# Performance work log

Measured on AMD Instinct MI355X. Metric: run time of the kernel, lower is better.

Reference implementation:

```python
import jax, jax.numpy as jnp
import numpy as np

B, C, L = 16, 64, 512
L_P = 16
D_MODEL = 1024
STRIDE = 8
N_P = (L - L_P) // STRIDE + 2  # 64 patches
PERIOD = L // 2                # statsmodels period = series_input_length / 2


def setup_inputs() -> dict:
    key = jax.random.key(0)
    ks = jax.random.split(key, 11)
    s = 0.02  # small init scale for weights
    return {
        "data_x": jax.random.normal(ks[0], (B, C, L), jnp.float32),
        "gamma": jax.random.uniform(ks[1], (B, C, L), jnp.float32),
        "beta": jax.random.uniform(ks[2], (B, C, L), jnp.float32),
        "w_trend": jax.random.normal(ks[3], (L_P, L), jnp.float32) * s,
        "b_trend": jax.random.normal(ks[4], (L_P,), jnp.float32) * s,
        "w_seasonal": jax.random.normal(ks[5], (L_P, L), jnp.float32) * s,
        "b_seasonal": jax.random.normal(ks[6], (L_P,), jnp.float32) * s,
        "w_resid": jax.random.normal(ks[7], (L_P, L), jnp.float32) * s,
        "b_resid": jax.random.normal(ks[8], (L_P,), jnp.float32) * s,
        "w_g": jax.random.normal(ks[9], (D_MODEL, 3 * L_P), jnp.float32) * s,
        "b_g": jax.random.normal(ks[10], (D_MODEL,), jnp.float32) * s,
    }


def _decompose(x):
    """Vectorized statsmodels seasonal_decompose(model='additive', period=L//2).

    trend: centered moving average with filter [0.5,1,...,1,0.5]/p (even period),
           NaN edges -> replaced by 0 (as in the torch module).
    seasonal: per-phase nanmean of detrended, demeaned, tiled to length L.
    resid: detrended - seasonal on the valid (non-NaN) region, 0 elsewhere.
    x: [B, C, L] -> (trend, seasonal, resid) each [B, C, L].
    """
    p = PERIOD
    filt = jnp.concatenate([jnp.full((1,), 0.5, x.dtype),
                            jnp.ones((p - 1,), x.dtype),
                            jnp.full((1,), 0.5, x.dtype)]) / p  # len p+1 (p even)
    head = p // 2               # leading NaN count (filter is symmetric)
    nvalid = L - p              # valid trend samples
    xf = x.reshape(B * C, 1, L)
    tv = jax.lax.conv_general_dilated(xf, filt.reshape(1, 1, p + 1),
                                      (1,), "VALID")[:, 0, :]  # [BC, L-p]
    trend = jnp.zeros((B * C, L), x.dtype).at[:, head:head + nvalid].set(tv)
    dv = x.reshape(B * C, L)[:, head:head + nvalid] - tv  # detrended, valid region
    # per-phase nanmean over valid detrended samples
    phase = (head + jnp.arange(nvalid)) % p               # phase of each valid index
    sums = jnp.zeros((B * C, p), x.dtype).at[:, phase].add(dv)
    counts = jnp.zeros((p,), x.dtype).at[phase].add(1.0)
    pa = sums / counts                                    # period averages [BC, p]
    pa = pa - jnp.mean(pa, axis=1, keepdims=True)
    seasonal = jnp.tile(pa, (1, L // p))                  # L = 2p exactly
    resid = jnp.zeros((B * C, L), x.dtype).at[:, head:head + nvalid].set(
        dv - seasonal[:, head:head + nvalid])
    return (trend.reshape(B, C, L), seasonal.reshape(B, C, L),
            resid.reshape(B, C, L))


def reference(data_x, gamma, beta, w_trend, b_trend, w_seasonal, b_seasonal,
              w_resid, b_resid, w_g, b_g):
    # 'transformed': per-channel stats (dim=1), torch var is unbiased (ddof=1), epsi=0
    mean = jnp.mean(data_x, axis=1)
    var = jnp.var(data_x, axis=1, ddof=1)
    mean = (mean / jnp.sqrt(var))[:, None, :]             # [B,1,L] broadcast over C
    x = gamma * (data_x - mean) + beta
    x = jax.lax.stop_gradient(x)                          # season() detaches
    trend, seasonal, resid = _decompose(x)
    t = trend @ w_trend.T + b_trend                       # [B,C,L_p]
    s = seasonal @ w_seasonal.T + b_seasonal
    r = resid @ w_resid.T + b_resid
    feats = jnp.concatenate([t, s, r], axis=-1)           # [B,C,3*L_p]
    feats = jnp.broadcast_to(feats[:, :, None, :], (B, C, N_P, 3 * L_P))
    return feats @ w_g.T + b_g                            # [B,C,N_p,D_MODEL]
```

## Files before the change

### kernel.cpp

```cpp
#include <hip/hip_runtime.h>
#include <math.h>

#define BB   16
#define CC   64
#define LL   512
#define LP   16
#define DM   1024
#define NP   64
#define PRD  256
#define HEAD 128
#define NV   256

typedef float f32x4 __attribute__((ext_vector_type(4)));

#define OFF_MEANP 0
#define OFF_WSF   8192
#define OFF_WRS   12288
#define OFF_WGT   12304

__global__ __launch_bounds__(256) void statsprep_kernel(
    const float* __restrict__ dx, const float* __restrict__ w_s,
    const float* __restrict__ w_r, const float* __restrict__ w_g,
    float* __restrict__ ws)
{
    const int tid = threadIdx.x, bid = blockIdx.x;
    if (bid < 32) {
        int id = bid * 256 + tid;
        int b = id >> 9, l = id & 511;
        const float* p = dx + (size_t)b * CC * LL + l;
        float s = 0.f, sq = 0.f;
#pragma unroll 8
        for (int c = 0; c < CC; ++c) {
            float v = p[(size_t)c * LL];
            s += v; sq += v * v;
        }
        float mean = s * (1.0f / CC);
        float var  = (sq - (float)CC * mean * mean) * (1.0f / (CC - 1));
        ws[OFF_MEANP + id] = mean / sqrtf(var);
    } else if (bid == 32) {
#pragma unroll
        for (int idx = tid; idx < 16 * PRD; idx += 256) {
            int g = idx >> 8, m = idx & 255;
            ws[OFF_WSF + idx] = w_s[g * LL + m] + w_s[g * LL + PRD + m];
        }
        int g = tid >> 4, ln = tid & 15;
        float s = 0.f;
        for (int k = ln; k < PRD; k += 16) s += w_r[g * LL + HEAD + k];
#pragma unroll
        for (int m = 8; m; m >>= 1) s += __shfl_xor(s, m, 16);
        if (ln == 0) ws[OFF_WRS + g] = s;
    } else {
        int base = (bid - 33) * 3072 + tid;
#pragma unroll
        for (int k = 0; k < 12; ++k) {
            int e = base + k * 256;
            int j = e >> 10, d = e & 1023;
            ws[OFF_WGT + e] = w_g[d * 48 + j];
        }
    }
}

__global__ __launch_bounds__(256) void fused_kernel(
    const float* __restrict__ dx,    const float* __restrict__ gamma,
    const float* __restrict__ beta,  const float* __restrict__ w_t,
    const float* __restrict__ b_t,   const float* __restrict__ b_s,
    const float* __restrict__ b_r,   const float* __restrict__ b_g,
    const float* __restrict__ ws,    float* __restrict__ out)
{
    __shared__ __align__(16) float xs[LL];
    __shared__ __align__(16) float pps[LL/2 + 1];
    __shared__ __align__(16) float tvs[NV];
    __shared__ __align__(16) float pas[PRD];
    __shared__ __align__(16) float feats[48];
    __shared__ __align__(16) float sres[DM];
    __shared__ float wsum[4];
    __shared__ float wred[4];

    const int tid  = threadIdx.x;
    const int lane = tid & 63;
    const int wv   = tid >> 6;
    const int bc   = blockIdx.x;
    const int b    = bc >> 6;

    const size_t base = (size_t)bc * LL;
    float2 xv = ((const float2*)(dx    + base))[tid];
    float2 gv = ((const float2*)(gamma + base))[tid];
    float2 bv = ((const float2*)(beta  + base))[tid];
    float2 mv = ((const float2*)(ws + OFF_MEANP + (size_t)b * LL))[tid];
    float2 xp;
    xp.x = gv.x * (xv.x - mv.x) + bv.x;
    xp.y = gv.y * (xv.y - mv.y) + bv.y;
    ((float2*)xs)[tid] = xp;

    float v = xp.x + xp.y;
#pragma unroll
    for (int d = 1; d < 64; d <<= 1) {
        float t = __shfl_up(v, d, 64);
        if (lane >= d) v += t;
    }
    if (lane == 63) wsum[wv] = v;
    __syncthreads();
    float off = 0.f;
    for (int w = 0; w < wv; ++w) off += wsum[w];
    pps[tid + 1] = v + off;
    if (tid == 0) pps[0] = 0.f;
    __syncthreads();

    const int i  = tid;
    const int k2 = i + 257;
    const float Pi = pps[i  >> 1] + ((i  & 1) ? xs[i  & ~1] : 0.f);
    const float Pk = pps[k2 >> 1] + ((k2 & 1) ? xs[k2 & ~1] : 0.f);
    const float tv = (Pk - Pi - 0.5f * (xs[i] + xs[i + 256])) * (1.0f / 256.0f);
    tvs[i] = tv;
    const float dv = xs[HEAD + i] - tv;

    float r = dv;
#pragma unroll
    for (int m = 32; m; m >>= 1) r += __shfl_xor(r, m, 64);
    if (lane == 0) wred[wv] = r;
    __syncthreads();
    const float mdv = (wred[0] + wred[1] + wred[2] + wred[3]) * (1.0f / 256.0f);

    pas[(i + 128) & 255] = dv - mdv;
    __syncthreads();

    {
        const int g  = tid >> 4;
        const int ln = tid & 15;
        const f32x4* wt4  = (const f32x4*)(w_t + g * LL + HEAD);
        const f32x4* wsf4 = (const f32x4*)(ws + OFF_WSF + g * PRD);
        const f32x4* tv4  = (const f32x4*)tvs;
        const f32x4* pa4  = (const f32x4*)pas;
        float at = 0.f, as = 0.f;
#pragma unroll
        for (int q = 0; q < 4; ++q) {
            const int m = ln * 4 + q;
            f32x4 t = tv4[m], p = pa4[m];
            f32x4 a = wt4[m], sfw = wsf4[m];
            at += t.x * a.x + t.y * a.y + t.z * a.z + t.w * a.w;
            as += p.x * sfw.x + p.y * sfw.y + p.z * sfw.z + p.w * sfw.w;
        }
#pragma unroll
        for (int msk = 8; msk; msk >>= 1) {
            at += __shfl_xor(at, msk, 64);
            as += __shfl_xor(as, msk, 64);
        }
        if (ln == 0) {
            feats[g]      = at + b_t[g];
            feats[16 + g] = as + b_s[g];
            feats[32 + g] = mdv * ws[OFF_WRS + g] + b_r[g];
        }
    }
    __syncthreads();

    const float* wT = ws + OFF_WGT;
    float acc0 = b_g[tid];
    float acc1 = b_g[256 + tid];
    float acc2 = b_g[512 + tid];
    float acc3 = b_g[768 + tid];
#pragma unroll
    for (int j = 0; j < 48; ++j) {
        const float fj = feats[j];
        const float* w = wT + j * DM + tid;
        acc0 = fmaf(fj, w[0],   acc0);
        acc1 = fmaf(fj, w[256], acc1);
        acc2 = fmaf(fj, w[512], acc2);
        acc3 = fmaf(fj, w[768], acc3);
    }
    sres[tid]       = acc0;
    sres[256 + tid] = acc1;
    sres[512 + tid] = acc2;
    sres[768 + tid] = acc3;
    __syncthreads();

    const f32x4 res = ((const f32x4*)sres)[tid];
    f32x4* op = (f32x4*)out + (size_t)bc * (NP * DM / 4) + tid;
#pragma unroll
    for (int n = 0; n < NP; ++n)
        op[(size_t)n * (DM / 4)] = res;
}

extern "C" void kernel_launch(void* const* d_in, const int* in_sizes, int n_in,
                              void* d_out, int out_size, void* d_ws, size_t ws_size,
                              hipStream_t stream) {
    const float* dx    = (const float*)d_in[0];
    const float* gamma = (const float*)d_in[1];
    const float* beta  = (const float*)d_in[2];
    const float* w_t   = (const float*)d_in[3];
    const float* b_t   = (const float*)d_in[4];
    const float* w_s   = (const float*)d_in[5];
    const float* b_s   = (const float*)d_in[6];
    const float* w_r   = (const float*)d_in[7];
    const float* b_r   = (const float*)d_in[8];
    const float* w_g   = (const float*)d_in[9];
    const float* b_g   = (const float*)d_in[10];
    float* out = (float*)d_out;
    float* ws  = (float*)d_ws;

    statsprep_kernel<<<49, 256, 0, stream>>>(dx, w_s, w_r, w_g, ws);
    fused_kernel<<<BB * CC, 256, 0, stream>>>(
        dx, gamma, beta, w_t, b_t, b_s, b_r, b_g, ws, out);
}
```

Baseline: 66.08 us.

## Split each row's output across four blocks with redundant feature computation

```diff
diff --git a/kernel.cpp b/kernel.cpp
--- a/kernel.cpp
+++ b/kernel.cpp
@@ -72,14 +72,15 @@
     __shared__ __align__(16) float tvs[NV];
     __shared__ __align__(16) float pas[PRD];
     __shared__ __align__(16) float feats[48];
-    __shared__ __align__(16) float sres[DM];
+    __shared__ __align__(16) float sres[256];
     __shared__ float wsum[4];
     __shared__ float wred[4];
 
     const int tid  = threadIdx.x;
     const int lane = tid & 63;
     const int wv   = tid >> 6;
-    const int bc   = blockIdx.x;
+    const int bc   = blockIdx.x >> 2;
+    const int q    = blockIdx.x & 3;
     const int b    = bc >> 6;
 
     const size_t base = (size_t)bc * LL;
@@ -133,8 +134,8 @@
         const f32x4* pa4  = (const f32x4*)pas;
         float at = 0.f, as = 0.f;
 #pragma unroll
-        for (int q = 0; q < 4; ++q) {
-            const int m = ln * 4 + q;
+        for (int qq = 0; qq < 4; ++qq) {
+            const int m = ln * 4 + qq;
             f32x4 t = tv4[m], p = pa4[m];
             f32x4 a = wt4[m], sfw = wsf4[m];
             at += t.x * a.x + t.y * a.y + t.z * a.z + t.w * a.w;
@@ -153,31 +154,21 @@
     }
     __syncthreads();
 
-    const float* wT = ws + OFF_WGT;
-    float acc0 = b_g[tid];
-    float acc1 = b_g[256 + tid];
-    float acc2 = b_g[512 + tid];
-    float acc3 = b_g[768 + tid];
+    const int d = q * 256 + tid;
+    const float* wT = ws + OFF_WGT + d;
+    float acc = b_g[d];
 #pragma unroll
-    for (int j = 0; j < 48; ++j) {
-        const float fj = feats[j];
-        const float* w = wT + j * DM + tid;
-        acc0 = fmaf(fj, w[0],   acc0);
-        acc1 = fmaf(fj, w[256], acc1);
-        acc2 = fmaf(fj, w[512], acc2);
-        acc3 = fmaf(fj, w[768], acc3);
-    }
-    sres[tid]       = acc0;
-    sres[256 + tid] = acc1;
-    sres[512 + tid] = acc2;
-    sres[768 + tid] = acc3;
+    for (int j = 0; j < 48; ++j)
+        acc = fmaf(feats[j], wT[j * DM], acc);
+    sres[tid] = acc;
     __syncthreads();
 
-    const f32x4 res = ((const f32x4*)sres)[tid];
-    f32x4* op = (f32x4*)out + (size_t)bc * (NP * DM / 4) + tid;
+    const f32x4 vv = ((const f32x4*)sres)[lane];
+    f32x4* op = (f32x4*)out + (size_t)bc * (NP * DM / 4)
+              + (size_t)(wv * 16) * (DM / 4) + q * 64 + lane;
 #pragma unroll
-    for (int n = 0; n < NP; ++n)
-        op[(size_t)n * (DM / 4)] = res;
+    for (int n = 0; n < 16; ++n)
+        op[n * (DM / 4)] = vv;
 }
 
 extern "C" void kernel_launch(void* const* d_in, const int* in_sizes, int n_in,
@@ -198,6 +189,6 @@
     float* ws  = (float*)d_ws;
 
     statsprep_kernel<<<49, 256, 0, stream>>>(dx, w_s, w_r, w_g, ws);
-    fused_kernel<<<BB * CC, 256, 0, stream>>>(
+    fused_kernel<<<BB * CC * 4, 256, 0, stream>>>(
         dx, gamma, beta, w_t, b_t, b_s, b_r, b_g, ws, out);
 }
```

Result: slower. 77.84 us (+17.8%).

## Fold per-batch channel stats and weight folding into fused kernel

Applied to the files above, without the earlier changes.

```diff
diff --git a/kernel.cpp b/kernel.cpp
--- a/kernel.cpp
+++ b/kernel.cpp
@@ -13,57 +13,26 @@
 
 typedef float f32x4 __attribute__((ext_vector_type(4)));
 
-#define OFF_MEANP 0
-#define OFF_WSF   8192
-#define OFF_WRS   12288
-#define OFF_WGT   12304
+#define OFF_WGT 0
 
-__global__ __launch_bounds__(256) void statsprep_kernel(
-    const float* __restrict__ dx, const float* __restrict__ w_s,
-    const float* __restrict__ w_r, const float* __restrict__ w_g,
-    float* __restrict__ ws)
+__global__ __launch_bounds__(256) void transpose_kernel(
+    const float* __restrict__ w_g, float* __restrict__ ws)
 {
     const int tid = threadIdx.x, bid = blockIdx.x;
-    if (bid < 32) {
-        int id = bid * 256 + tid;
-        int b = id >> 9, l = id & 511;
-        const float* p = dx + (size_t)b * CC * LL + l;
-        float s = 0.f, sq = 0.f;
-#pragma unroll 8
-        for (int c = 0; c < CC; ++c) {
-            float v = p[(size_t)c * LL];
-            s += v; sq += v * v;
-        }
-        float mean = s * (1.0f / CC);
-        float var  = (sq - (float)CC * mean * mean) * (1.0f / (CC - 1));
-        ws[OFF_MEANP + id] = mean / sqrtf(var);
-    } else if (bid == 32) {
+    int base = bid * 3072 + tid;
 #pragma unroll
-        for (int idx = tid; idx < 16 * PRD; idx += 256) {
-            int g = idx >> 8, m = idx & 255;
-            ws[OFF_WSF + idx] = w_s[g * LL + m] + w_s[g * LL + PRD + m];
-        }
-        int g = tid >> 4, ln = tid & 15;
-        float s = 0.f;
-        for (int k = ln; k < PRD; k += 16) s += w_r[g * LL + HEAD + k];
-#pragma unroll
-        for (int m = 8; m; m >>= 1) s += __shfl_xor(s, m, 16);
-        if (ln == 0) ws[OFF_WRS + g] = s;
-    } else {
-        int base = (bid - 33) * 3072 + tid;
-#pragma unroll
-        for (int k = 0; k < 12; ++k) {
-            int e = base + k * 256;
-            int j = e >> 10, d = e & 1023;
-            ws[OFF_WGT + e] = w_g[d * 48 + j];
-        }
+    for (int k = 0; k < 12; ++k) {
+        int e = base + k * 256;
+        int j = e >> 10, d = e & 1023;
+        ws[OFF_WGT + e] = w_g[d * 48 + j];
     }
 }
 
 __global__ __launch_bounds__(256) void fused_kernel(
     const float* __restrict__ dx,    const float* __restrict__ gamma,
     const float* __restrict__ beta,  const float* __restrict__ w_t,
-    const float* __restrict__ b_t,   const float* __restrict__ b_s,
+    const float* __restrict__ b_t,   const float* __restrict__ w_s,
+    const float* __restrict__ b_s,   const float* __restrict__ w_r,
     const float* __restrict__ b_r,   const float* __restrict__ b_g,
     const float* __restrict__ ws,    float* __restrict__ out)
 {
@@ -72,7 +41,6 @@
     __shared__ __align__(16) float tvs[NV];
     __shared__ __align__(16) float pas[PRD];
     __shared__ __align__(16) float feats[48];
-    __shared__ __align__(16) float sres[DM];
     __shared__ float wsum[4];
     __shared__ float wred[4];
 
@@ -81,15 +49,33 @@
     const int wv   = tid >> 6;
     const int bc   = blockIdx.x;
     const int b    = bc >> 6;
+    const int cown = bc & 63;
+
+    const float2* dxb = (const float2*)(dx + (size_t)b * CC * LL);
+    float2 sv = make_float2(0.f, 0.f), qv = make_float2(0.f, 0.f);
+    float2 xv = make_float2(0.f, 0.f);
+#pragma unroll 8
+    for (int c = 0; c < CC; ++c) {
+        float2 v = dxb[c * 256 + tid];
+        if (c == cown) xv = v;
+        sv.x += v.x;       sv.y += v.y;
+        qv.x += v.x * v.x; qv.y += v.y * v.y;
+    }
+    float2 mp;
+    {
+        float mx = sv.x * (1.0f / CC), my = sv.y * (1.0f / CC);
+        float vx = (qv.x - (float)CC * mx * mx) * (1.0f / (CC - 1));
+        float vy = (qv.y - (float)CC * my * my) * (1.0f / (CC - 1));
+        mp.x = mx / sqrtf(vx);
+        mp.y = my / sqrtf(vy);
+    }
 
     const size_t base = (size_t)bc * LL;
-    float2 xv = ((const float2*)(dx    + base))[tid];
     float2 gv = ((const float2*)(gamma + base))[tid];
     float2 bv = ((const float2*)(beta  + base))[tid];
-    float2 mv = ((const float2*)(ws + OFF_MEANP + (size_t)b * LL))[tid];
     float2 xp;
-    xp.x = gv.x * (xv.x - mv.x) + bv.x;
-    xp.y = gv.y * (xv.y - mv.y) + bv.y;
+    xp.x = gv.x * (xv.x - mp.x) + bv.x;
+    xp.y = gv.y * (xv.y - mp.y) + bv.y;
     ((float2*)xs)[tid] = xp;
 
     float v = xp.x + xp.y;
@@ -128,56 +114,48 @@
         const int g  = tid >> 4;
         const int ln = tid & 15;
         const f32x4* wt4  = (const f32x4*)(w_t + g * LL + HEAD);
-        const f32x4* wsf4 = (const f32x4*)(ws + OFF_WSF + g * PRD);
+        const f32x4* ws4a = (const f32x4*)(w_s + g * LL);
+        const f32x4* ws4b = (const f32x4*)(w_s + g * LL + PRD);
+        const f32x4* wr4  = (const f32x4*)(w_r + g * LL + HEAD);
         const f32x4* tv4  = (const f32x4*)tvs;
         const f32x4* pa4  = (const f32x4*)pas;
-        float at = 0.f, as = 0.f;
+        float at = 0.f, as = 0.f, ar = 0.f;
 #pragma unroll
         for (int q = 0; q < 4; ++q) {
             const int m = ln * 4 + q;
-            f32x4 t = tv4[m], p = pa4[m];
-            f32x4 a = wt4[m], sfw = wsf4[m];
+            f32x4 t  = tv4[m],  p  = pa4[m];
+            f32x4 a  = wt4[m];
+            f32x4 s1 = ws4a[m], s2 = ws4b[m];
+            f32x4 rr = wr4[m];
             at += t.x * a.x + t.y * a.y + t.z * a.z + t.w * a.w;
-            as += p.x * sfw.x + p.y * sfw.y + p.z * sfw.z + p.w * sfw.w;
+            as += p.x * (s1.x + s2.x) + p.y * (s1.y + s2.y)
+                + p.z * (s1.z + s2.z) + p.w * (s1.w + s2.w);
+            ar += rr.x + rr.y + rr.z + rr.w;
         }
 #pragma unroll
         for (int msk = 8; msk; msk >>= 1) {
             at += __shfl_xor(at, msk, 64);
             as += __shfl_xor(as, msk, 64);
+            ar += __shfl_xor(ar, msk, 64);
         }
         if (ln == 0) {
             feats[g]      = at + b_t[g];
             feats[16 + g] = as + b_s[g];
-            feats[32 + g] = mdv * ws[OFF_WRS + g] + b_r[g];
+            feats[32 + g] = mdv * ar + b_r[g];
         }
     }
     __syncthreads();
 
-    const float* wT = ws + OFF_WGT;
-    float acc0 = b_g[tid];
-    float acc1 = b_g[256 + tid];
-    float acc2 = b_g[512 + tid];
-    float acc3 = b_g[768 + tid];
+    const f32x4* wT4 = (const f32x4*)(ws + OFF_WGT);
+    f32x4 acc = ((const f32x4*)b_g)[tid];
 #pragma unroll
-    for (int j = 0; j < 48; ++j) {
-        const float fj = feats[j];
-        const float* w = wT + j * DM + tid;
-        acc0 = fmaf(fj, w[0],   acc0);
-        acc1 = fmaf(fj, w[256], acc1);
-        acc2 = fmaf(fj, w[512], acc2);
-        acc3 = fmaf(fj, w[768], acc3);
-    }
-    sres[tid]       = acc0;
-    sres[256 + tid] = acc1;
-    sres[512 + tid] = acc2;
-    sres[768 + tid] = acc3;
-    __syncthreads();
+    for (int j = 0; j < 48; ++j)
+        acc += feats[j] * wT4[j * 256 + tid];
 
-    const f32x4 res = ((const f32x4*)sres)[tid];
     f32x4* op = (f32x4*)out + (size_t)bc * (NP * DM / 4) + tid;
 #pragma unroll
     for (int n = 0; n < NP; ++n)
-        op[(size_t)n * (DM / 4)] = res;
+        op[(size_t)n * (DM / 4)] = acc;
 }
 
 extern "C" void kernel_launch(void* const* d_in, const int* in_sizes, int n_in,
@@ -197,7 +175,7 @@
     float* out = (float*)d_out;
     float* ws  = (float*)d_ws;
 
-    statsprep_kernel<<<49, 256, 0, stream>>>(dx, w_s, w_r, w_g, ws);
+    transpose_kernel<<<16, 256, 0, stream>>>(w_g, ws);
     fused_kernel<<<BB * CC, 256, 0, stream>>>(
-        dx, gamma, beta, w_t, b_t, b_s, b_r, b_g, ws, out);
+        dx, gamma, beta, w_t, b_t, w_s, b_s, w_r, b_r, b_g, ws, out);
 }
```

Measured after the change: 66.68 us. Within noise of the previous version (+0.9%).
